# Optimization experiments

Hardware: AMD Instinct MI355X
Metric: run time of the kernel (lower is better)

## Reference

```python
import jax, jax.numpy as jnp
import numpy as np

N = 131072      # active sparse voxels (N_in == N_out, stride=1)
K = 27          # 3^3 kernel offsets
CIN = 64
COUT = 128
BN_EPS = 1e-5
NEG_SLOPE = 0.01  # MinkowskiLeakyReLU default


def setup_inputs() -> dict:
    key = jax.random.key(0)
    k1, k2, k3, k4 = jax.random.split(key, 4)
    feats = jax.random.normal(k1, (N, CIN), dtype=jnp.float32)
    neighbor_idx = jax.random.randint(k2, (N, K), 0, N, dtype=jnp.int32)
    neighbor_mask = jax.random.randint(k3, (N, K), 0, 2, dtype=jnp.int32).astype(jnp.bool_)
    W = jax.random.normal(k4, (K, CIN, COUT), dtype=jnp.float32) * (1.0 / np.sqrt(K * CIN))
    gamma = jnp.ones((COUT,), dtype=jnp.float32)
    beta = jnp.zeros((COUT,), dtype=jnp.float32)
    return {"feats": feats, "neighbor_idx": neighbor_idx,
            "neighbor_mask": neighbor_mask, "W": W, "gamma": gamma, "beta": beta}


def _sparse_conv(feats, neighbor_idx, neighbor_mask, W):
    # gather-GEMM-scatter, accumulated over the K kernel offsets via scan
    # to avoid materializing the [N, K, CIN] gathered tensor.
    idx_k = neighbor_idx.T          # [K, N]
    mask_k = neighbor_mask.T        # [K, N]

    def step(acc, xs):
        Wk, ik, mk = xs             # [CIN,COUT], [N], [N]
        g = feats[ik] * mk.astype(feats.dtype)[:, None]   # [N, CIN]
        return acc + g @ Wk, None

    acc0 = jnp.zeros((feats.shape[0], W.shape[-1]), dtype=feats.dtype)
    out, _ = jax.lax.scan(step, acc0, (W, idx_k, mask_k))
    return out                      # [N, COUT]


def reference(feats, neighbor_idx, neighbor_mask, W, gamma, beta):
    y = _sparse_conv(feats, neighbor_idx, neighbor_mask, W)
    # MinkowskiBatchNorm: per-channel stats over all sparse points (train mode)
    mean = jnp.mean(y, axis=0)
    var = jnp.var(y, axis=0)
    y = (y - mean) * jax.lax.rsqrt(var + BN_EPS) * gamma + beta
    # MinkowskiLeakyReLU
    return jnp.where(y > 0, y, NEG_SLOPE * y)
```

## Files before the change

kernel.cpp:

```cpp
#include <hip/hip_runtime.h>
#include <hip/hip_bf16.h>

#define NPTS 131072
#define K 27
#define CIN 64
#define COUT 128
#define BM 128

constexpr float BN_EPS = 1e-5f;
constexpr float NEG_SLOPE = 0.01f;

typedef __attribute__((ext_vector_type(8))) short short8;
typedef __attribute__((ext_vector_type(4))) float f32x4;

__device__ inline unsigned int pk_bf16(float a, float b) {
    __hip_bfloat16 ha = __float2bfloat16(a), hb = __float2bfloat16(b);
    unsigned short ua = *reinterpret_cast<unsigned short*>(&ha);
    unsigned short ub = *reinterpret_cast<unsigned short*>(&hb);
    return (unsigned int)ua | ((unsigned int)ub << 16);
}
__device__ inline unsigned short bf16_bits(float a) {
    __hip_bfloat16 h = __float2bfloat16(a);
    return *reinterpret_cast<unsigned short*>(&h);
}

__global__ __launch_bounds__(256) void prep_all(
    const float* __restrict__ feats, const float* __restrict__ W,
    const int* __restrict__ nidx, const int* __restrict__ nmask,
    unsigned short* __restrict__ featsb, unsigned short* __restrict__ Wt,
    int* __restrict__ midx, int do_midx)
{
    size_t t = (size_t)blockIdx.x * 256 + threadIdx.x;

    {
        const float4* src = (const float4*)(feats) + t * 2;
        float4 v0 = src[0], v1 = src[1];
        uint4 o;
        o.x = pk_bf16(v0.x, v0.y); o.y = pk_bf16(v0.z, v0.w);
        o.z = pk_bf16(v1.x, v1.y); o.w = pk_bf16(v1.z, v1.w);
        ((uint4*)featsb)[t] = o;
    }
    if (t < (size_t)K * COUT * CIN) {
        int k  = (int)(t / (COUT * CIN));
        int r  = (int)(t % (COUT * CIN));
        int co = r / CIN;
        int ci = r % CIN;
        Wt[t] = bf16_bits(W[(k * CIN + ci) * COUT + co]);
    }
    if (do_midx && t < (size_t)(NPTS * K / 4)) {
        int4 iv = ((const int4*)nidx)[t];
        int4 mv = ((const int4*)nmask)[t];
        int4 o;
        o.x = mv.x ? iv.x : NPTS;
        o.y = mv.y ? iv.y : NPTS;
        o.z = mv.z ? iv.z : NPTS;
        o.w = mv.w ? iv.w : NPTS;
        ((int4*)midx)[t] = o;
    }
}

template<bool MIDX, bool YB>
__global__ __launch_bounds__(512) void conv_kernel(
    const unsigned short* __restrict__ featsb,
    const int* __restrict__ midx,
    const int* __restrict__ nidx,
    const int* __restrict__ nmask,
    const unsigned short* __restrict__ Wt,
    float* __restrict__ y,
    unsigned short* __restrict__ ybf,
    float* __restrict__ accum)
{
    __shared__ unsigned char Alds[BM * 128];
    __shared__ unsigned char Blds[COUT * 128];

    const int tid  = threadIdx.x;
    const int l    = tid & 63;
    const int wid  = tid >> 6;
    const int wr   = wid >> 1;
    const int wc   = wid & 1;
    const int base = blockIdx.x * BM;

    const int arow = tid >> 2;
    const int aq   = tid & 3;
    const int bcol = tid >> 2;
    const int bq   = tid & 3;

    auto loadIdx = [&](int kq) -> int {
        kq = kq < K ? kq : K - 1;
        int o = (base + arow) * K + kq;
        if constexpr (MIDX) return midx[o];
        else                return nmask[o] ? nidx[o] : NPTS;
    };

    const int aswz = (arow & 7) << 4;
    unsigned char* ap = Alds + arow * 128;
    const int bswz = (bcol & 7) << 4;
    unsigned char* bp = Blds + bcol * 128;

    uint4 a0, a1, b0, b1;
    int   id_nxt;

#define ISSUE_A(id)                                                           \
    { const uint4* p_ = (const uint4*)(featsb + (size_t)(id) * CIN) + aq * 2; \
      a0 = p_[0]; a1 = p_[1]; }
#define ISSUE_B(kq)                                                           \
    { const uint4* p_ = (const uint4*)(Wt + ((size_t)(kq) * COUT + bcol) * CIN) + bq * 2; \
      b0 = p_[0]; b1 = p_[1]; }
#define WRITE_AB()                                                            \
    { *(uint4*)(ap + ((aq * 32 +  0) ^ aswz)) = a0;                           \
      *(uint4*)(ap + ((aq * 32 + 16) ^ aswz)) = a1;                           \
      *(uint4*)(bp + ((bq * 32 +  0) ^ bswz)) = b0;                           \
      *(uint4*)(bp + ((bq * 32 + 16) ^ bswz)) = b1; }

    f32x4 acc[2][4];
#pragma unroll
    for (int m = 0; m < 2; ++m)
#pragma unroll
        for (int n = 0; n < 4; ++n) acc[m][n] = (f32x4)0.f;

#define MFMA_TILE()                                                           \
    _Pragma("unroll")                                                         \
    for (int ks = 0; ks < 2; ++ks) {                                          \
        const int kbyte = ks * 64 + (l >> 4) * 16;                            \
        short8 afr[2], bfr[4];                                                \
        _Pragma("unroll")                                                     \
        for (int m = 0; m < 2; ++m) {                                         \
            int row = wr * 32 + m * 16 + (l & 15);                            \
            afr[m] = *(const short8*)(Alds + row * 128                        \
                        + (kbyte ^ ((row & 7) << 4)));                        \
        }                                                                     \
        _Pragma("unroll")                                                     \
        for (int n = 0; n < 4; ++n) {                                         \
            int col = wc * 64 + n * 16 + (l & 15);                            \
            bfr[n] = *(const short8*)(Blds + col * 128                        \
                        + (kbyte ^ ((col & 7) << 4)));                        \
        }                                                                     \
        _Pragma("unroll")                                                     \
        for (int m = 0; m < 2; ++m)                                           \
            _Pragma("unroll")                                                 \
            for (int n = 0; n < 4; ++n)                                       \
                acc[m][n] = __builtin_amdgcn_mfma_f32_16x16x32_bf16(          \
                    afr[m], bfr[n], acc[m][n], 0, 0, 0);                      \
    }

    {
        int id0 = loadIdx(0);
        ISSUE_A(id0);
        ISSUE_B(0);
        id_nxt = loadIdx(1);
    }

    for (int k = 0; k < K; ++k) {
        __syncthreads();
        WRITE_AB();
        if (k + 1 < K) {
            ISSUE_A(id_nxt);
            ISSUE_B(k + 1);
            id_nxt = loadIdx(k + 2);
        }
        __syncthreads();
        MFMA_TILE();
    }

#pragma unroll
    for (int m = 0; m < 2; ++m)
#pragma unroll
        for (int n = 0; n < 4; ++n) {
            int gcol = wc * 64 + n * 16 + (l & 15);
#pragma unroll
            for (int r = 0; r < 4; ++r) {
                int grow = base + wr * 32 + m * 16 + (l >> 4) * 4 + r;
                if constexpr (YB) {
                    __builtin_nontemporal_store(bf16_bits(acc[m][n][r]),
                        &ybf[(size_t)grow * COUT + gcol]);
                } else {
                    __builtin_nontemporal_store(acc[m][n][r],
                        &y[(size_t)grow * COUT + gcol]);
                }
            }
        }

    float sv[4], s2v[4];
#pragma unroll
    for (int n = 0; n < 4; ++n) {
        float s = 0.f, s2 = 0.f;
#pragma unroll
        for (int m = 0; m < 2; ++m)
#pragma unroll
            for (int r = 0; r < 4; ++r) { float v = acc[m][n][r]; s += v; s2 += v * v; }
        s  += __shfl_xor(s, 16);  s  += __shfl_xor(s, 32);
        s2 += __shfl_xor(s2, 16); s2 += __shfl_xor(s2, 32);
        sv[n] = s; s2v[n] = s2;
    }
    __syncthreads();
    float* statf = (float*)Alds;
    if (l < 16) {
#pragma unroll
        for (int n = 0; n < 4; ++n) {
            int c = wc * 64 + n * 16 + l;
            statf[(0 * 4 + wr) * 128 + c] = sv[n];
            statf[(1 * 4 + wr) * 128 + c] = s2v[n];
        }
    }
    __syncthreads();
    if (tid < 128) {
        float s  = statf[0 * 128 + tid] + statf[1 * 128 + tid]
                 + statf[2 * 128 + tid] + statf[3 * 128 + tid];
        float s2 = statf[4 * 128 + tid] + statf[5 * 128 + tid]
                 + statf[6 * 128 + tid] + statf[7 * 128 + tid];
        atomicAdd(&accum[tid], s);
        atomicAdd(&accum[128 + tid], s2);
    }
#undef ISSUE_A
#undef ISSUE_B
#undef WRITE_AB
#undef MFMA_TILE
}

__global__ void finalize_kernel(const float* __restrict__ accum,
                                const float* __restrict__ gamma,
                                const float* __restrict__ beta,
                                float* __restrict__ sb)
{
    int c = threadIdx.x;
    float invN  = 1.0f / (float)NPTS;
    float mean  = accum[c] * invN;
    float var   = accum[128 + c] * invN - mean * mean;
    float scale = gamma[c] * rsqrtf(var + BN_EPS);
    sb[c]       = scale;
    sb[128 + c] = beta[c] - mean * scale;
}

template<bool YB>
__global__ __launch_bounds__(256) void bn_kernel(
    const unsigned short* __restrict__ ybf, float* __restrict__ y,
    const float* __restrict__ sb)
{
    size_t start = (size_t)blockIdx.x * blockDim.x + threadIdx.x;
    const size_t step = (size_t)gridDim.x * blockDim.x;
    if constexpr (YB) {
        int c0 = (int)((start * 8) & (COUT - 1));
        float sc[8], bi[8];
#pragma unroll
        for (int j = 0; j < 8; ++j) { sc[j] = sb[c0 + j]; bi[j] = sb[COUT + c0 + j]; }
        const size_t total = (size_t)NPTS * COUT / 8;
        for (size_t idx = start; idx < total; idx += step) {
            uint4 u = ((const uint4*)ybf)[idx];
            unsigned int uu[4] = {u.x, u.y, u.z, u.w};
            float o[8];
#pragma unroll
            for (int j = 0; j < 4; ++j) {
                float vlo = __uint_as_float(uu[j] << 16);
                float vhi = __uint_as_float(uu[j] & 0xffff0000u);
                float a = vlo * sc[2*j]   + bi[2*j];
                float b = vhi * sc[2*j+1] + bi[2*j+1];
                o[2*j]   = a > 0.f ? a : NEG_SLOPE * a;
                o[2*j+1] = b > 0.f ? b : NEG_SLOPE * b;
            }
            float4* dst = (float4*)(y + idx * 8);
            dst[0] = make_float4(o[0], o[1], o[2], o[3]);
            dst[1] = make_float4(o[4], o[5], o[6], o[7]);
        }
    } else {
        int c0 = (int)((start * 4) & (COUT - 1));
        float sc[4], bi[4];
#pragma unroll
        for (int j = 0; j < 4; ++j) { sc[j] = sb[c0 + j]; bi[j] = sb[COUT + c0 + j]; }
        const size_t total = (size_t)NPTS * COUT / 4;
        for (size_t idx = start; idx < total; idx += step) {
            float4 v = ((const float4*)y)[idx];
            v.x = v.x * sc[0] + bi[0]; v.x = v.x > 0.f ? v.x : NEG_SLOPE * v.x;
            v.y = v.y * sc[1] + bi[1]; v.y = v.y > 0.f ? v.y : NEG_SLOPE * v.y;
            v.z = v.z * sc[2] + bi[2]; v.z = v.z > 0.f ? v.z : NEG_SLOPE * v.z;
            v.w = v.w * sc[3] + bi[3]; v.w = v.w > 0.f ? v.w : NEG_SLOPE * v.w;
            ((float4*)y)[idx] = v;
        }
    }
}

extern "C" void kernel_launch(void* const* d_in, const int* in_sizes, int n_in,
                              void* d_out, int out_size, void* d_ws, size_t ws_size,
                              hipStream_t stream)
{
    const float* feats = (const float*)d_in[0];
    const int*   nidx  = (const int*)d_in[1];
    const int*   nmask = (const int*)d_in[2];
    const float* W     = (const float*)d_in[3];
    const float* gamma = (const float*)d_in[4];
    const float* beta  = (const float*)d_in[5];

    float* y = (float*)d_out;

    float*          accum  = (float*)d_ws;
    float*          sb     = (float*)((char*)d_ws + 1024);
    unsigned short* Wt     = (unsigned short*)((char*)d_ws + 4096);
    unsigned short* featsb = (unsigned short*)((char*)d_ws + 458752);
    int*            midx   = (int*)((char*)d_ws + 17236224);
    unsigned short* ybf    = (unsigned short*)((char*)d_ws + 31494144);
    const size_t need_midx = 31494144;
    const size_t need_ybf  = 31494144 + (size_t)NPTS * COUT * 2;
    const bool use_midx = ws_size >= need_midx;
    const bool use_ybf  = ws_size >= need_ybf;

    hipMemsetAsync(accum, 0, 2 * COUT * sizeof(float), stream);
    hipMemsetAsync(featsb + (size_t)NPTS * CIN, 0, CIN * 2, stream);

    prep_all<<<4096, 256, 0, stream>>>(feats, W, nidx, nmask,
                                       featsb, Wt, midx, (int)use_midx);

    if (use_midx && use_ybf)
        conv_kernel<true, true ><<<NPTS / BM, 512, 0, stream>>>(featsb, midx, nidx, nmask, Wt, y, ybf, accum);
    else if (use_midx)
        conv_kernel<true, false><<<NPTS / BM, 512, 0, stream>>>(featsb, midx, nidx, nmask, Wt, y, ybf, accum);
    else
        conv_kernel<false, false><<<NPTS / BM, 512, 0, stream>>>(featsb, midx, nidx, nmask, Wt, y, ybf, accum);

    finalize_kernel<<<1, 128, 0, stream>>>(accum, gamma, beta, sb);

    if (use_midx && use_ybf)
        bn_kernel<true ><<<2048, 256, 0, stream>>>(ybf, y, sb);
    else
        bn_kernel<false><<<2048, 256, 0, stream>>>(ybf, y, sb);
}
```

Before: 121.8 us.

## Fuse conv, BN and LeakyReLU with a cooperative grid-wide sync

Adds a cooperative kernel that runs the gather-GEMM, accumulates per-channel BN statistics through atomics, then does a grid-wide sync. After the sync it computes scale and bias and applies BN plus LeakyReLU directly to the register accumulators before writing y once. This removes the bf16 intermediate store and reload and the separate finalize and BN launches. In exchange, every block must be co-resident: the 1024 blocks of 512 threads need four blocks per CU, which constrains register use via launch bounds and may cause spills. If the occupancy check reports fewer than four blocks per CU, it falls back to the old multi-kernel path.

```diff
diff --git a/kernel.cpp b/kernel.cpp
--- a/kernel.cpp
+++ b/kernel.cpp
@@ -1,5 +1,8 @@
 #include <hip/hip_runtime.h>
 #include <hip/hip_bf16.h>
+#include <hip/hip_cooperative_groups.h>
+
+namespace cg = cooperative_groups;
 
 #define NPTS 131072
 #define K 27
@@ -59,6 +62,157 @@
     }
 }
 
+#define CONV_BODY_COMMON(LOADIDX_EXPR)                                        \
+    __shared__ unsigned char Alds[BM * 128];                       \
+    __shared__ unsigned char Blds[COUT * 128];                     \
+    const int tid  = threadIdx.x;                                             \
+    const int l    = tid & 63;                                                \
+    const int wid  = tid >> 6;                                                \
+    const int wr   = wid >> 1;                                                \
+    const int wc   = wid & 1;                                                 \
+    const int base = blockIdx.x * BM;                                         \
+    const int arow = tid >> 2;                                                \
+    const int aq   = tid & 3;                                                 \
+    const int bcol = tid >> 2;                                                \
+    const int bq   = tid & 3;                                                 \
+    auto loadIdx = [&](int kq) -> int {                                       \
+        kq = kq < K ? kq : K - 1;                                             \
+        int o = (base + arow) * K + kq;                                       \
+        return LOADIDX_EXPR;                                                  \
+    };                                                                        \
+    const int aswz = (arow & 7) << 4;                                         \
+    unsigned char* ap = Alds + arow * 128;                                    \
+    const int bswz = (bcol & 7) << 4;                                         \
+    unsigned char* bp = Blds + bcol * 128;                                    \
+    uint4 a0, a1, b0, b1;                                                     \
+    int   id_nxt;                                                             \
+    f32x4 acc[2][4];                                                          \
+    _Pragma("unroll")                                                         \
+    for (int m = 0; m < 2; ++m)                                               \
+        _Pragma("unroll")                                                     \
+        for (int n = 0; n < 4; ++n) acc[m][n] = (f32x4)0.f;                   \
+    {                                                                         \
+        int id0 = loadIdx(0);                                                 \
+        const uint4* pa = (const uint4*)(featsb + (size_t)id0 * CIN) + aq * 2;\
+        a0 = pa[0]; a1 = pa[1];                                               \
+        const uint4* pb = (const uint4*)(Wt + (size_t)bcol * CIN) + bq * 2;   \
+        b0 = pb[0]; b1 = pb[1];                                               \
+        id_nxt = loadIdx(1);                                                  \
+    }                                                                         \
+    for (int k = 0; k < K; ++k) {                                             \
+        __syncthreads();                                                      \
+        *(uint4*)(ap + ((aq * 32 +  0) ^ aswz)) = a0;                         \
+        *(uint4*)(ap + ((aq * 32 + 16) ^ aswz)) = a1;                         \
+        *(uint4*)(bp + ((bq * 32 +  0) ^ bswz)) = b0;                         \
+        *(uint4*)(bp + ((bq * 32 + 16) ^ bswz)) = b1;                         \
+        if (k + 1 < K) {                                                      \
+            const uint4* pa = (const uint4*)(featsb + (size_t)id_nxt * CIN) + aq * 2; \
+            a0 = pa[0]; a1 = pa[1];                                           \
+            const uint4* pb = (const uint4*)(Wt + ((size_t)(k + 1) * COUT + bcol) * CIN) + bq * 2; \
+            b0 = pb[0]; b1 = pb[1];                                           \
+            id_nxt = loadIdx(k + 2);                                          \
+        }                                                                     \
+        __syncthreads();                                                      \
+        _Pragma("unroll")                                                     \
+        for (int ks = 0; ks < 2; ++ks) {                                      \
+            const int kbyte = ks * 64 + (l >> 4) * 16;                        \
+            short8 afr[2], bfr[4];                                            \
+            _Pragma("unroll")                                                 \
+            for (int m = 0; m < 2; ++m) {                                     \
+                int row = wr * 32 + m * 16 + (l & 15);                        \
+                afr[m] = *(const short8*)(Alds + row * 128                    \
+                            + (kbyte ^ ((row & 7) << 4)));                    \
+            }                                                                 \
+            _Pragma("unroll")                                                 \
+            for (int n = 0; n < 4; ++n) {                                     \
+                int col = wc * 64 + n * 16 + (l & 15);                        \
+                bfr[n] = *(const short8*)(Blds + col * 128                    \
+                            + (kbyte ^ ((col & 7) << 4)));                    \
+            }                                                                 \
+            _Pragma("unroll")                                                 \
+            for (int m = 0; m < 2; ++m)                                       \
+                _Pragma("unroll")                                             \
+                for (int n = 0; n < 4; ++n)                                   \
+                    acc[m][n] = __builtin_amdgcn_mfma_f32_16x16x32_bf16(      \
+                        afr[m], bfr[n], acc[m][n], 0, 0, 0);                  \
+        }                                                                     \
+    }                                                                         \
+                                                      \
+    float sv[4], s2v[4];                                                      \
+    _Pragma("unroll")                                                         \
+    for (int n = 0; n < 4; ++n) {                                             \
+        float s = 0.f, s2 = 0.f;                                              \
+        _Pragma("unroll")                                                     \
+        for (int m = 0; m < 2; ++m)                                           \
+            _Pragma("unroll")                                                 \
+            for (int r = 0; r < 4; ++r) { float v = acc[m][n][r]; s += v; s2 += v * v; } \
+        s  += __shfl_xor(s, 16);  s  += __shfl_xor(s, 32);                    \
+        s2 += __shfl_xor(s2, 16); s2 += __shfl_xor(s2, 32);                   \
+        sv[n] = s; s2v[n] = s2;                                               \
+    }                                                                         \
+    __syncthreads();                                                          \
+    float* statf = (float*)Alds;                                              \
+    if (l < 16) {                                                             \
+        _Pragma("unroll")                                                     \
+        for (int n = 0; n < 4; ++n) {                                         \
+            int c = wc * 64 + n * 16 + l;                                     \
+            statf[(0 * 4 + wr) * 128 + c] = sv[n];                            \
+            statf[(1 * 4 + wr) * 128 + c] = s2v[n];                           \
+        }                                                                     \
+    }                                                                         \
+    __syncthreads();                                                          \
+    if (tid < 128) {                                                          \
+        float s  = statf[0 * 128 + tid] + statf[1 * 128 + tid]               \
+                 + statf[2 * 128 + tid] + statf[3 * 128 + tid];              \
+        float s2 = statf[4 * 128 + tid] + statf[5 * 128 + tid]               \
+                 + statf[6 * 128 + tid] + statf[7 * 128 + tid];              \
+        atomicAdd(&accum[tid], s);                                            \
+        atomicAdd(&accum[128 + tid], s2);                                     \
+    }
+
+__global__ __launch_bounds__(512, 8) void conv_fused(
+    const unsigned short* __restrict__ featsb,
+    const int* __restrict__ midx,
+    const unsigned short* __restrict__ Wt,
+    float* __restrict__ y,
+    const float* __restrict__ gamma,
+    const float* __restrict__ beta,
+    float* accum)
+{
+    CONV_BODY_COMMON(midx[o])
+
+    cg::this_grid().sync();
+
+    float* sbuf = (float*)Blds;
+    if (tid < 128) {
+        const volatile float* ac = (const volatile float*)accum;
+        float invN  = 1.0f / (float)NPTS;
+        float s     = ac[tid];
+        float s2    = ac[128 + tid];
+        float mean  = s * invN;
+        float var   = s2 * invN - mean * mean;
+        float scale = gamma[tid] * rsqrtf(var + BN_EPS);
+        sbuf[tid]       = scale;
+        sbuf[128 + tid] = beta[tid] - mean * scale;
+    }
+    __syncthreads();
+
+#pragma unroll
+    for (int m = 0; m < 2; ++m)
+#pragma unroll
+        for (int n = 0; n < 4; ++n) {
+            int gcol = wc * 64 + n * 16 + (l & 15);
+            float sc = sbuf[gcol], bi = sbuf[128 + gcol];
+#pragma unroll
+            for (int r = 0; r < 4; ++r) {
+                int grow = base + wr * 32 + m * 16 + (l >> 4) * 4 + r;
+                float v = acc[m][n][r] * sc + bi;
+                v = v > 0.f ? v : NEG_SLOPE * v;
+                __builtin_nontemporal_store(v, &y[(size_t)grow * COUT + gcol]);
+            }
+        }
+}
+
 template<bool MIDX, bool YB>
 __global__ __launch_bounds__(512) void conv_kernel(
     const unsigned short* __restrict__ featsb,
@@ -68,99 +222,9 @@
     const unsigned short* __restrict__ Wt,
     float* __restrict__ y,
     unsigned short* __restrict__ ybf,
-    float* __restrict__ accum)
-{
-    __shared__ unsigned char Alds[BM * 128];
-    __shared__ unsigned char Blds[COUT * 128];
-
-    const int tid  = threadIdx.x;
-    const int l    = tid & 63;
-    const int wid  = tid >> 6;
-    const int wr   = wid >> 1;
-    const int wc   = wid & 1;
-    const int base = blockIdx.x * BM;
-
-    const int arow = tid >> 2;
-    const int aq   = tid & 3;
-    const int bcol = tid >> 2;
-    const int bq   = tid & 3;
-
-    auto loadIdx = [&](int kq) -> int {
-        kq = kq < K ? kq : K - 1;
-        int o = (base + arow) * K + kq;
-        if constexpr (MIDX) return midx[o];
-        else                return nmask[o] ? nidx[o] : NPTS;
-    };
-
-    const int aswz = (arow & 7) << 4;
-    unsigned char* ap = Alds + arow * 128;
-    const int bswz = (bcol & 7) << 4;
-    unsigned char* bp = Blds + bcol * 128;
-
-    uint4 a0, a1, b0, b1;
-    int   id_nxt;
-
-#define ISSUE_A(id)                                                           \
-    { const uint4* p_ = (const uint4*)(featsb + (size_t)(id) * CIN) + aq * 2; \
-      a0 = p_[0]; a1 = p_[1]; }
-#define ISSUE_B(kq)                                                           \
-    { const uint4* p_ = (const uint4*)(Wt + ((size_t)(kq) * COUT + bcol) * CIN) + bq * 2; \
-      b0 = p_[0]; b1 = p_[1]; }
-#define WRITE_AB()                                                            \
-    { *(uint4*)(ap + ((aq * 32 +  0) ^ aswz)) = a0;                           \
-      *(uint4*)(ap + ((aq * 32 + 16) ^ aswz)) = a1;                           \
-      *(uint4*)(bp + ((bq * 32 +  0) ^ bswz)) = b0;                           \
-      *(uint4*)(bp + ((bq * 32 + 16) ^ bswz)) = b1; }
-
-    f32x4 acc[2][4];
-#pragma unroll
-    for (int m = 0; m < 2; ++m)
-#pragma unroll
-        for (int n = 0; n < 4; ++n) acc[m][n] = (f32x4)0.f;
-
-#define MFMA_TILE()                                                           \
-    _Pragma("unroll")                                                         \
-    for (int ks = 0; ks < 2; ++ks) {                                          \
-        const int kbyte = ks * 64 + (l >> 4) * 16;                            \
-        short8 afr[2], bfr[4];                                                \
-        _Pragma("unroll")                                                     \
-        for (int m = 0; m < 2; ++m) {                                         \
-            int row = wr * 32 + m * 16 + (l & 15);                            \
-            afr[m] = *(const short8*)(Alds + row * 128                        \
-                        + (kbyte ^ ((row & 7) << 4)));                        \
-        }                                                                     \
-        _Pragma("unroll")                                                     \
-        for (int n = 0; n < 4; ++n) {                                         \
-            int col = wc * 64 + n * 16 + (l & 15);                            \
-            bfr[n] = *(const short8*)(Blds + col * 128                        \
-                        + (kbyte ^ ((col & 7) << 4)));                        \
-        }                                                                     \
-        _Pragma("unroll")                                                     \
-        for (int m = 0; m < 2; ++m)                                           \
-            _Pragma("unroll")                                                 \
-            for (int n = 0; n < 4; ++n)                                       \
-                acc[m][n] = __builtin_amdgcn_mfma_f32_16x16x32_bf16(          \
-                    afr[m], bfr[n], acc[m][n], 0, 0, 0);                      \
-    }
-
-    {
-        int id0 = loadIdx(0);
-        ISSUE_A(id0);
-        ISSUE_B(0);
-        id_nxt = loadIdx(1);
-    }
-
-    for (int k = 0; k < K; ++k) {
-        __syncthreads();
-        WRITE_AB();
-        if (k + 1 < K) {
-            ISSUE_A(id_nxt);
-            ISSUE_B(k + 1);
-            id_nxt = loadIdx(k + 2);
-        }
-        __syncthreads();
-        MFMA_TILE();
-    }
+    float* accum)
+{
+    CONV_BODY_COMMON((MIDX ? midx[o] : (nmask[o] ? nidx[o] : NPTS)))
 
 #pragma unroll
     for (int m = 0; m < 2; ++m)
@@ -179,42 +243,6 @@
                 }
             }
         }
-
-    float sv[4], s2v[4];
-#pragma unroll
-    for (int n = 0; n < 4; ++n) {
-        float s = 0.f, s2 = 0.f;
-#pragma unroll
-        for (int m = 0; m < 2; ++m)
-#pragma unroll
-            for (int r = 0; r < 4; ++r) { float v = acc[m][n][r]; s += v; s2 += v * v; }
-        s  += __shfl_xor(s, 16);  s  += __shfl_xor(s, 32);
-        s2 += __shfl_xor(s2, 16); s2 += __shfl_xor(s2, 32);
-        sv[n] = s; s2v[n] = s2;
-    }
-    __syncthreads();
-    float* statf = (float*)Alds;
-    if (l < 16) {
-#pragma unroll
-        for (int n = 0; n < 4; ++n) {
-            int c = wc * 64 + n * 16 + l;
-            statf[(0 * 4 + wr) * 128 + c] = sv[n];
-            statf[(1 * 4 + wr) * 128 + c] = s2v[n];
-        }
-    }
-    __syncthreads();
-    if (tid < 128) {
-        float s  = statf[0 * 128 + tid] + statf[1 * 128 + tid]
-                 + statf[2 * 128 + tid] + statf[3 * 128 + tid];
-        float s2 = statf[4 * 128 + tid] + statf[5 * 128 + tid]
-                 + statf[6 * 128 + tid] + statf[7 * 128 + tid];
-        atomicAdd(&accum[tid], s);
-        atomicAdd(&accum[128 + tid], s2);
-    }
-#undef ISSUE_A
-#undef ISSUE_B
-#undef WRITE_AB
-#undef MFMA_TILE
 }
 
 __global__ void finalize_kernel(const float* __restrict__ accum,
@@ -302,11 +330,27 @@
     const bool use_midx = ws_size >= need_midx;
     const bool use_ybf  = ws_size >= need_ybf;
 
+    int maxb = 0;
+    bool coop = use_midx;
+    if (coop) {
+        if (hipOccupancyMaxActiveBlocksPerMultiprocessor(
+                &maxb, conv_fused, 512, 0) != hipSuccess || maxb < 4)
+            coop = false;
+    }
+
     hipMemsetAsync(accum, 0, 2 * COUT * sizeof(float), stream);
     hipMemsetAsync(featsb + (size_t)NPTS * CIN, 0, CIN * 2, stream);
 
     prep_all<<<4096, 256, 0, stream>>>(feats, W, nidx, nmask,
                                        featsb, Wt, midx, (int)use_midx);
+
+    if (coop) {
+        void* args[] = {(void*)&featsb, (void*)&midx, (void*)&Wt, (void*)&y,
+                        (void*)&gamma, (void*)&beta, (void*)&accum};
+        hipLaunchCooperativeKernel((const void*)conv_fused,
+                                   dim3(NPTS / BM), dim3(512), args, 0, stream);
+        return;
+    }
 
     if (use_midx && use_ybf)
         conv_kernel<true, true ><<<NPTS / BM, 512, 0, stream>>>(featsb, midx, nidx, nmask, Wt, y, ybf, accum);
```

Result: slower. 125.9 us (+3.4%).
